# Performance work log

Hardware: AMD Instinct MI355X
Metric: run time of the kernel (lower is better)

The kernel has to match this reference:

```python
import math
import jax, jax.numpy as jnp
import numpy as np

N_HEADS = 16
D_EMBED = 1024
D_HEAD = D_EMBED // N_HEADS


def setup_inputs() -> dict:
    key = jax.random.key(0)
    k1, k2, k3, k4, k5 = jax.random.split(key, 5)
    B, S, D = 4, 2048, D_EMBED
    scale = 1.0 / math.sqrt(D)
    return {
        "x": jax.random.normal(k1, (B, S, D), dtype=jnp.float32),
        "in_proj_w": jax.random.normal(k2, (3 * D, D), dtype=jnp.float32) * scale,
        "in_proj_b": jax.random.normal(k3, (3 * D,), dtype=jnp.float32) * 0.02,
        "out_proj_w": jax.random.normal(k4, (D, D), dtype=jnp.float32) * scale,
        "out_proj_b": jax.random.normal(k5, (D,), dtype=jnp.float32) * 0.02,
        "causal_mask": 0,
    }


def reference(x, in_proj_w, in_proj_b, out_proj_w, out_proj_b, causal_mask):
    B, S, D = x.shape
    # in_proj: torch Linear -> x @ W^T + b, then chunk into q,k,v
    qkv = x @ in_proj_w.T + in_proj_b              # [B,S,3D]
    q, k, v = jnp.split(qkv, 3, axis=-1)
    # [B,S,D] -> [B,H,S,d]
    def heads(t):
        return t.reshape(B, S, N_HEADS, D_HEAD).transpose(0, 2, 1, 3)
    q, k, v = heads(q), heads(k), heads(v)
    weight = jnp.einsum("bhsd,bhtd->bhst", q, k)   # [B,H,S,S] materialized scores
    if causal_mask:
        mask = jnp.triu(jnp.ones((S, S), dtype=bool), k=1)
        weight = jnp.where(mask, -jnp.inf, weight)
    weight = jax.nn.softmax(weight / math.sqrt(D_HEAD), axis=-1)
    out = jnp.einsum("bhst,bhtd->bhsd", weight, v)  # [B,H,S,d]
    out = out.transpose(0, 2, 1, 3).reshape(B, S, D)
    return out @ out_proj_w.T + out_proj_b
```

## Files before the change

kernel.cpp:

```cpp
#include <hip/hip_runtime.h>

typedef unsigned short u16;
typedef _Float16 h8 __attribute__((ext_vector_type(8)));
typedef __fp16 fp16x2 __attribute__((ext_vector_type(2)));
typedef float f32x4 __attribute__((ext_vector_type(4)));

constexpr int B_ = 4, S_ = 2048, D_ = 1024, H_ = 16;

__device__ __forceinline__ void async16(const void* g, void* l) {
  __builtin_amdgcn_global_load_lds(
      (const __attribute__((address_space(1))) void*)g,
      (__attribute__((address_space(3))) void*)l, 16, 0, 0);
}

__device__ __forceinline__ unsigned pk2(float a, float b) {
  union { fp16x2 h; unsigned u; } c;
  c.h = __builtin_amdgcn_cvt_pkrtz(a, b);
  return c.u;
}

__global__ __launch_bounds__(256) void cvt_kernel(
    const float* __restrict__ src, _Float16* __restrict__ dst, int n)
{
  const int i = (blockIdx.x * 256 + threadIdx.x) * 4;
  if (i >= n) return;
  const float4 v = *(const float4*)(src + i);
  uint2 o;
  o.x = pk2(v.x, v.y);
  o.y = pk2(v.z, v.w);
  *(uint2*)(dst + i) = o;
}

template<bool OUT_HALF>
__global__ __launch_bounds__(256, 2) void gemm_wide(
    const _Float16* __restrict__ A, const _Float16* __restrict__ Bw,
    const float* __restrict__ bias, void* __restrict__ Cout,
    int M, int N, int K)
{
  __shared__ __align__(16) _Float16 sA[2][4096];
  __shared__ __align__(16) _Float16 sB[2][8192];

  const int tid = threadIdx.x;
  const int lane = tid & 63, w = tid >> 6;
  const int wm = w & 1, wn = w >> 1;
  const int m0 = blockIdx.y * 128, n0 = blockIdx.x * 256;

  const int sr = 16 * w + (lane & 15);
  const int ss = lane >> 4;
  const _Float16* gA1 = A + (size_t)(m0 + sr) * K + 8 * ss;
  const _Float16* gA2 = gA1 + (size_t)64 * K;
  const _Float16* gB1 = Bw + (size_t)(n0 + sr) * K + 8 * ss;

  const f32x4 zf = {0.f, 0.f, 0.f, 0.f};
  f32x4 acc[4][8];
#pragma unroll
  for (int i = 0; i < 4; ++i)
#pragma unroll
    for (int j = 0; j < 8; ++j) acc[i][j] = zf;

  async16(gA1, &sA[0][w * 512]);
  async16(gA2, &sA[0][(w + 4) * 512]);
#pragma unroll
  for (int t = 0; t < 4; ++t)
    async16(gB1 + (size_t)(64 * t) * K, &sB[0][(w + 4 * t) * 512]);

  const int NIT = K >> 5;
  for (int it = 0; it < NIT; ++it) {
    const int cur = it & 1;
    __syncthreads();
    if (it + 1 < NIT) {
      const int kn = (it + 1) << 5;
      async16(gA1 + kn, &sA[cur ^ 1][w * 512]);
      async16(gA2 + kn, &sA[cur ^ 1][(w + 4) * 512]);
#pragma unroll
      for (int t = 0; t < 4; ++t)
        async16(gB1 + (size_t)(64 * t) * K + kn, &sB[cur ^ 1][(w + 4 * t) * 512]);
    }

    h8 fa[4], fb[8];
#pragma unroll
    for (int i = 0; i < 4; ++i)
      fa[i] = *(const h8*)&sA[cur][((wm * 4 + i) << 9) + (lane << 3)];
#pragma unroll
    for (int j = 0; j < 8; ++j)
      fb[j] = *(const h8*)&sB[cur][((wn * 8 + j) << 9) + (lane << 3)];
#pragma unroll
    for (int i = 0; i < 4; ++i)
#pragma unroll
      for (int j = 0; j < 8; ++j)
        acc[i][j] = __builtin_amdgcn_mfma_f32_16x16x32_f16(fa[i], fb[j], acc[i][j], 0, 0, 0);
  }

  const int g = lane >> 4, cc = lane & 15;
#pragma unroll
  for (int j = 0; j < 8; ++j) {
    const int col = n0 + (wn * 8 + j) * 16 + cc;
    const float bv = bias[col];
#pragma unroll
    for (int i = 0; i < 4; ++i) {
      const int rowb = m0 + (wm * 4 + i) * 16 + g * 4;
#pragma unroll
      for (int r = 0; r < 4; ++r) {
        const float v = acc[i][j][r] + bv;
        if constexpr (OUT_HALF)
          ((_Float16*)Cout)[(size_t)(rowb + r) * N + col] = (_Float16)v;
        else
          ((float*)Cout)[(size_t)(rowb + r) * N + col] = v;
      }
    }
  }
}

template<bool OUT_HALF>
__global__ __launch_bounds__(256) void gemm_f16(
    const _Float16* __restrict__ A, const _Float16* __restrict__ Bw,
    const float* __restrict__ bias, void* __restrict__ Cout,
    int M, int N, int K)
{
  __shared__ __align__(16) _Float16 sA[2][4096];
  __shared__ __align__(16) _Float16 sB[2][4096];

  const int tid = threadIdx.x;
  const int lane = tid & 63, w = tid >> 6;
  const int wm = w & 1, wn = w >> 1;
  const int m0 = blockIdx.y * 128, n0 = blockIdx.x * 128;

  const int sr = 16 * w + (lane & 15);
  const int ss = lane >> 4;
  const _Float16* gA1 = A + (size_t)(m0 + sr) * K + 8 * ss;
  const _Float16* gA2 = gA1 + (size_t)64 * K;
  const _Float16* gB1 = Bw + (size_t)(n0 + sr) * K + 8 * ss;
  const _Float16* gB2 = gB1 + (size_t)64 * K;

  const f32x4 zf = {0.f, 0.f, 0.f, 0.f};
  f32x4 acc[4][4];
#pragma unroll
  for (int i = 0; i < 4; ++i)
#pragma unroll
    for (int j = 0; j < 4; ++j) acc[i][j] = zf;

  async16(gA1, &sA[0][w * 512]);
  async16(gA2, &sA[0][(w + 4) * 512]);
  async16(gB1, &sB[0][w * 512]);
  async16(gB2, &sB[0][(w + 4) * 512]);

  const int NIT = K >> 5;
  for (int it = 0; it < NIT; ++it) {
    const int cur = it & 1;
    __syncthreads();
    if (it + 1 < NIT) {
      const int kn = (it + 1) << 5;
      async16(gA1 + kn, &sA[cur ^ 1][w * 512]);
      async16(gA2 + kn, &sA[cur ^ 1][(w + 4) * 512]);
      async16(gB1 + kn, &sB[cur ^ 1][w * 512]);
      async16(gB2 + kn, &sB[cur ^ 1][(w + 4) * 512]);
    }

    h8 fa[4], fb[4];
#pragma unroll
    for (int i = 0; i < 4; ++i) {
      fa[i] = *(const h8*)&sA[cur][((wm * 4 + i) << 9) + (lane << 3)];
      fb[i] = *(const h8*)&sB[cur][((wn * 4 + i) << 9) + (lane << 3)];
    }
#pragma unroll
    for (int i = 0; i < 4; ++i)
#pragma unroll
      for (int j = 0; j < 4; ++j)
        acc[i][j] = __builtin_amdgcn_mfma_f32_16x16x32_f16(fa[i], fb[j], acc[i][j], 0, 0, 0);
  }

  const int g = lane >> 4, cc = lane & 15;
#pragma unroll
  for (int j = 0; j < 4; ++j) {
    const int col = n0 + (wn * 4 + j) * 16 + cc;
    const float bv = bias[col];
#pragma unroll
    for (int i = 0; i < 4; ++i) {
      const int rowb = m0 + (wm * 4 + i) * 16 + g * 4;
#pragma unroll
      for (int r = 0; r < 4; ++r) {
        const float v = acc[i][j][r] + bv;
        if constexpr (OUT_HALF)
          ((_Float16*)Cout)[(size_t)(rowb + r) * N + col] = (_Float16)v;
        else
          ((float*)Cout)[(size_t)(rowb + r) * N + col] = v;
      }
    }
  }
}

__global__ __launch_bounds__(256) void transpose_v(
    const u16* __restrict__ qkv, u16* __restrict__ vT)
{
  __shared__ u16 T[64 * 73];
  const int tid = threadIdx.x;
  const int bh = blockIdx.y, s0 = blockIdx.x * 64;
  const int b = bh >> 4, h = bh & 15;
#pragma unroll
  for (int t = 0; t < 2; ++t) {
    const int c = tid + t * 256, r = c >> 3, cs = c & 7;
    union { int4 v; u16 s[8]; } u;
    u.v = *(const int4*)(qkv + (size_t)(b * S_ + s0 + r) * 3072 + 2048 + h * 64 + 8 * cs);
#pragma unroll
    for (int i = 0; i < 8; ++i) T[r * 73 + 8 * cs + i] = u.s[i];
  }
  __syncthreads();
#pragma unroll
  for (int t = 0; t < 2; ++t) {
    const int c = tid + t * 256, rd = c >> 3, ss = c & 7;
    union { int4 v; u16 s[8]; } u;
#pragma unroll
    for (int i = 0; i < 8; ++i) u.s[i] = T[(8 * ss + i) * 73 + rd];
    *(int4*)(vT + (size_t)(bh * 64 + rd) * S_ + s0 + 8 * ss) = u.v;
  }
}

__global__ __launch_bounds__(128, 2) void attn_f16(
    const _Float16* __restrict__ qkv, const _Float16* __restrict__ vT,
    _Float16* __restrict__ attnO, const int* __restrict__ causal_ptr)
{
  __shared__ __align__(16) _Float16 sQP[9216];
  __shared__ __align__(16) _Float16 sK[4096];
  __shared__ __align__(16) _Float16 sV[4096];

  const int tid = threadIdx.x, lane = tid & 63, w = tid >> 6;
  const int q4 = lane >> 4, cc = lane & 15;
  const int bh = blockIdx.y, b = bh >> 4, h = bh & 15;
  const int q0 = blockIdx.x * 128;
  const int causal = causal_ptr[0];

  const int rr = lane & 15, sc8 = lane >> 4;

#pragma unroll
  for (int tt = 0; tt < 4; ++tt) {
    const int t = 4 * w + tt;
#pragma unroll
    for (int sh = 0; sh < 2; ++sh) {
      const _Float16* g = qkv + (size_t)(b * S_ + q0 + 16 * t + rr) * 3072 + h * 64 + 8 * (4 * sh + sc8);
      async16(g, &sQP[t * 1024 + sh * 512]);
    }
  }
  __syncthreads();

  h8 qf[4][2];
#pragma unroll
  for (int m = 0; m < 4; ++m)
#pragma unroll
    for (int kk = 0; kk < 2; ++kk) {
      h8 v = *(const h8*)&sQP[((4 * w + m) << 10) + (kk << 9) + (lane << 3)];
      qf[m][kk] = v * (_Float16)0.18033688f;
    }

  h8 ones;
#pragma unroll
  for (int i = 0; i < 8; ++i) ones[i] = (_Float16)1.0f;

  const int wp = w * 4608;

  const f32x4 zf = {0.f, 0.f, 0.f, 0.f};
  f32x4 oa[4][4], lac[4];
#pragma unroll
  for (int m = 0; m < 4; ++m) {
    lac[m] = zf;
#pragma unroll
    for (int nt = 0; nt < 4; ++nt) oa[m][nt] = zf;
  }

  const int nit = causal ? (q0 / 64 + 2) : (S_ / 64);

  for (int it = 0; it < nit; ++it) {
    const int j0 = it * 64;
    __syncthreads();
#pragma unroll
    for (int tt = 0; tt < 2; ++tt) {
      const int t = 2 * w + tt;
#pragma unroll
      for (int sh = 0; sh < 2; ++sh) {
        const _Float16* gk = qkv + (size_t)(b * S_ + j0 + 16 * t + rr) * 3072 + 1024 + h * 64 + 8 * (4 * sh + sc8);
        const _Float16* gv = vT + (size_t)(bh * 64 + 16 * t + rr) * S_ + j0 + 8 * (4 * sh + sc8);
        async16(gk, &sK[t * 1024 + sh * 512]);
        async16(gv, &sV[t * 1024 + sh * 512]);
      }
    }
    __syncthreads();

#pragma unroll
    for (int nt = 0; nt < 4; ++nt) {
      const h8 kf0 = *(const h8*)&sK[(nt << 10) + (lane << 3)];
      const h8 kf1 = *(const h8*)&sK[(nt << 10) + 512 + (lane << 3)];
      f32x4 sc[4];
#pragma unroll
      for (int m = 0; m < 4; ++m) {
        sc[m] = __builtin_amdgcn_mfma_f32_16x16x32_f16(kf0, qf[m][0], zf, 0, 0, 0);
        sc[m] = __builtin_amdgcn_mfma_f32_16x16x32_f16(kf1, qf[m][1], sc[m], 0, 0, 0);
      }
      if (causal) {
#pragma unroll
        for (int m = 0; m < 4; ++m)
#pragma unroll
          for (int r = 0; r < 4; ++r)
            if ((j0 + nt * 16 + q4 * 4 + r) > (q0 + 64 * w + m * 16 + cc))
              sc[m][r] = -1.0e30f;
      }
#pragma unroll
      for (int m = 0; m < 4; ++m) {
        uint2 pk;
        pk.x = pk2(exp2f(sc[m][0]), exp2f(sc[m][1]));
        pk.y = pk2(exp2f(sc[m][2]), exp2f(sc[m][3]));
        *(uint2*)&sQP[wp + (m * 16 + cc) * 72 + nt * 16 + q4 * 4] = pk;
      }
    }

    asm volatile("s_waitcnt lgkmcnt(0)" ::: "memory");

    h8 pf0[4], pf1[4];
#pragma unroll
    for (int m = 0; m < 4; ++m) {
      pf0[m] = *(const h8*)&sQP[wp + (m * 16 + cc) * 72 + q4 * 8];
      pf1[m] = *(const h8*)&sQP[wp + (m * 16 + cc) * 72 + 32 + q4 * 8];
    }

#pragma unroll
    for (int m = 0; m < 4; ++m) {
      lac[m] = __builtin_amdgcn_mfma_f32_16x16x32_f16(pf0[m], ones, lac[m], 0, 0, 0);
      lac[m] = __builtin_amdgcn_mfma_f32_16x16x32_f16(pf1[m], ones, lac[m], 0, 0, 0);
    }
#pragma unroll
    for (int nt = 0; nt < 4; ++nt) {
      const h8 vf0 = *(const h8*)&sV[(nt << 10) + (lane << 3)];
      const h8 vf1 = *(const h8*)&sV[(nt << 10) + 512 + (lane << 3)];
#pragma unroll
      for (int m = 0; m < 4; ++m) {
        oa[m][nt] = __builtin_amdgcn_mfma_f32_16x16x32_f16(pf0[m], vf0, oa[m][nt], 0, 0, 0);
        oa[m][nt] = __builtin_amdgcn_mfma_f32_16x16x32_f16(pf1[m], vf1, oa[m][nt], 0, 0, 0);
      }
    }
  }

#pragma unroll
  for (int m = 0; m < 4; ++m) {
    float inv[4];
#pragma unroll
    for (int r = 0; r < 4; ++r) inv[r] = 1.0f / lac[m][r];
#pragma unroll
    for (int nt = 0; nt < 4; ++nt) {
      const int col = h * 64 + nt * 16 + cc;
#pragma unroll
      for (int r = 0; r < 4; ++r) {
        const int row = b * S_ + q0 + 64 * w + m * 16 + q4 * 4 + r;
        attnO[(size_t)row * D_ + col] = (_Float16)(oa[m][nt][r] * inv[r]);
      }
    }
  }
}

extern "C" void kernel_launch(void* const* d_in, const int* in_sizes, int n_in,
                              void* d_out, int out_size, void* d_ws, size_t ws_size,
                              hipStream_t stream)
{
  const float* x  = (const float*)d_in[0];
  const float* wi = (const float*)d_in[1];
  const float* bi = (const float*)d_in[2];
  const float* wo = (const float*)d_in[3];
  const float* bo = (const float*)d_in[4];
  const int* causal = (const int*)d_in[5];

  _Float16* xh   = (_Float16*)d_ws;
  _Float16* wih  = xh + 8388608;
  _Float16* woh  = wih + 3145728;
  _Float16* qkvb = woh + 1048576;
  _Float16* vT   = qkvb + 25165824;
  _Float16* attn = vT + 8388608;

  const int M = B_ * S_;

  cvt_kernel<<<8192, 256, 0, stream>>>(x, xh, M * D_);
  cvt_kernel<<<3072, 256, 0, stream>>>(wi, wih, 3 * D_ * D_);
  cvt_kernel<<<1024, 256, 0, stream>>>(wo, woh, D_ * D_);

  gemm_wide<true><<<dim3(12, 64), 256, 0, stream>>>(
      xh, wih, bi, qkvb, M, 3 * D_, D_);

  transpose_v<<<dim3(32, 64), 256, 0, stream>>>((const u16*)qkvb, (u16*)vT);

  attn_f16<<<dim3(16, 64), 128, 0, stream>>>(qkvb, vT, attn, causal);

  gemm_f16<false><<<dim3(8, 64), 256, 0, stream>>>(
      attn, woh, bo, d_out, M, D_, D_);
}
```

Baseline: 356.0 us.

## Widen attention blocks to 256 queries and merge fp32-to-fp16 conversion kernels

Attention blocks now use four waves over 256 queries instead of two waves over 128, so each K/V tile staged in LDS is shared by twice as many queries. Each wave loads one K/V subtile per iteration, and Q is read straight from global memory into registers instead of going through LDS. The three conversion launches are merged into one kernel that selects its source by index range, cutting launch overhead. Costs are fewer blocks in flight (512), larger P scratch in LDS, and a tighter occupancy target of three blocks per CU.

```diff
diff --git a/kernel.cpp b/kernel.cpp
--- a/kernel.cpp
+++ b/kernel.cpp
@@ -19,16 +19,21 @@
   return c.u;
 }
 
-__global__ __launch_bounds__(256) void cvt_kernel(
-    const float* __restrict__ src, _Float16* __restrict__ dst, int n)
+__global__ __launch_bounds__(256) void cvt3_kernel(
+    const float* __restrict__ x, const float* __restrict__ wi,
+    const float* __restrict__ wo, _Float16* __restrict__ xh,
+    _Float16* __restrict__ wih, _Float16* __restrict__ woh)
 {
   const int i = (blockIdx.x * 256 + threadIdx.x) * 4;
-  if (i >= n) return;
-  const float4 v = *(const float4*)(src + i);
+  const float* s; _Float16* d; int off;
+  if (i < 8388608)       { s = x;  d = xh;  off = i; }
+  else if (i < 11534336) { s = wi; d = wih; off = i - 8388608; }
+  else                   { s = wo; d = woh; off = i - 11534336; }
+  const float4 v = *(const float4*)(s + off);
   uint2 o;
   o.x = pk2(v.x, v.y);
   o.y = pk2(v.z, v.w);
-  *(uint2*)(dst + i) = o;
+  *(uint2*)(d + off) = o;
 }
 
 template<bool OUT_HALF>
@@ -215,40 +220,30 @@
   }
 }
 
-__global__ __launch_bounds__(128, 2) void attn_f16(
+__global__ __launch_bounds__(256, 3) void attn_f16(
     const _Float16* __restrict__ qkv, const _Float16* __restrict__ vT,
     _Float16* __restrict__ attnO, const int* __restrict__ causal_ptr)
 {
-  __shared__ __align__(16) _Float16 sQP[9216];
+  __shared__ __align__(16) _Float16 sP[18432];
   __shared__ __align__(16) _Float16 sK[4096];
   __shared__ __align__(16) _Float16 sV[4096];
 
   const int tid = threadIdx.x, lane = tid & 63, w = tid >> 6;
   const int q4 = lane >> 4, cc = lane & 15;
   const int bh = blockIdx.y, b = bh >> 4, h = bh & 15;
-  const int q0 = blockIdx.x * 128;
+  const int q0 = blockIdx.x * 256;
   const int causal = causal_ptr[0];
 
   const int rr = lane & 15, sc8 = lane >> 4;
 
-#pragma unroll
-  for (int tt = 0; tt < 4; ++tt) {
-    const int t = 4 * w + tt;
-#pragma unroll
-    for (int sh = 0; sh < 2; ++sh) {
-      const _Float16* g = qkv + (size_t)(b * S_ + q0 + 16 * t + rr) * 3072 + h * 64 + 8 * (4 * sh + sc8);
-      async16(g, &sQP[t * 1024 + sh * 512]);
-    }
-  }
-  __syncthreads();
-
   h8 qf[4][2];
 #pragma unroll
   for (int m = 0; m < 4; ++m)
 #pragma unroll
     for (int kk = 0; kk < 2; ++kk) {
-      h8 v = *(const h8*)&sQP[((4 * w + m) << 10) + (kk << 9) + (lane << 3)];
-      qf[m][kk] = v * (_Float16)0.18033688f;
+      const _Float16* gq = qkv + (size_t)(b * S_ + q0 + 64 * w + 16 * m + cc) * 3072
+                         + h * 64 + kk * 32 + 8 * q4;
+      qf[m][kk] = *(const h8*)gq * (_Float16)0.18033688f;
     }
 
   h8 ones;
@@ -266,22 +261,18 @@
     for (int nt = 0; nt < 4; ++nt) oa[m][nt] = zf;
   }
 
-  const int nit = causal ? (q0 / 64 + 2) : (S_ / 64);
+  const _Float16* gK = qkv + (size_t)(b * S_ + 16 * w + rr) * 3072 + 1024 + h * 64 + 8 * sc8;
+  const _Float16* gV = vT + ((size_t)bh * 64 + 16 * w + rr) * S_ + 8 * sc8;
+
+  const int nit = causal ? (q0 / 64 + 4) : (S_ / 64);
 
   for (int it = 0; it < nit; ++it) {
     const int j0 = it * 64;
     __syncthreads();
-#pragma unroll
-    for (int tt = 0; tt < 2; ++tt) {
-      const int t = 2 * w + tt;
-#pragma unroll
-      for (int sh = 0; sh < 2; ++sh) {
-        const _Float16* gk = qkv + (size_t)(b * S_ + j0 + 16 * t + rr) * 3072 + 1024 + h * 64 + 8 * (4 * sh + sc8);
-        const _Float16* gv = vT + (size_t)(bh * 64 + 16 * t + rr) * S_ + j0 + 8 * (4 * sh + sc8);
-        async16(gk, &sK[t * 1024 + sh * 512]);
-        async16(gv, &sV[t * 1024 + sh * 512]);
-      }
-    }
+    async16(gK + (size_t)j0 * 3072, &sK[w * 1024]);
+    async16(gK + (size_t)j0 * 3072 + 32, &sK[w * 1024 + 512]);
+    async16(gV + j0, &sV[w * 1024]);
+    async16(gV + j0 + 32, &sV[w * 1024 + 512]);
     __syncthreads();
 
 #pragma unroll
@@ -307,7 +298,7 @@
         uint2 pk;
         pk.x = pk2(exp2f(sc[m][0]), exp2f(sc[m][1]));
         pk.y = pk2(exp2f(sc[m][2]), exp2f(sc[m][3]));
-        *(uint2*)&sQP[wp + (m * 16 + cc) * 72 + nt * 16 + q4 * 4] = pk;
+        *(uint2*)&sP[wp + (m * 16 + cc) * 72 + nt * 16 + q4 * 4] = pk;
       }
     }
 
@@ -316,8 +307,8 @@
     h8 pf0[4], pf1[4];
 #pragma unroll
     for (int m = 0; m < 4; ++m) {
-      pf0[m] = *(const h8*)&sQP[wp + (m * 16 + cc) * 72 + q4 * 8];
-      pf1[m] = *(const h8*)&sQP[wp + (m * 16 + cc) * 72 + 32 + q4 * 8];
+      pf0[m] = *(const h8*)&sP[wp + (m * 16 + cc) * 72 + q4 * 8];
+      pf1[m] = *(const h8*)&sP[wp + (m * 16 + cc) * 72 + 32 + q4 * 8];
     }
 
 #pragma unroll
@@ -374,16 +365,14 @@
 
   const int M = B_ * S_;
 
-  cvt_kernel<<<8192, 256, 0, stream>>>(x, xh, M * D_);
-  cvt_kernel<<<3072, 256, 0, stream>>>(wi, wih, 3 * D_ * D_);
-  cvt_kernel<<<1024, 256, 0, stream>>>(wo, woh, D_ * D_);
+  cvt3_kernel<<<12288, 256, 0, stream>>>(x, wi, wo, xh, wih, woh);
 
   gemm_wide<true><<<dim3(12, 64), 256, 0, stream>>>(
       xh, wih, bi, qkvb, M, 3 * D_, D_);
 
   transpose_v<<<dim3(32, 64), 256, 0, stream>>>((const u16*)qkvb, (u16*)vT);
 
-  attn_f16<<<dim3(16, 64), 128, 0, stream>>>(qkvb, vT, attn, causal);
+  attn_f16<<<dim3(8, 64), 256, 0, stream>>>(qkvb, vT, attn, causal);
 
   gemm_f16<false><<<dim3(8, 64), 256, 0, stream>>>(
       attn, woh, bo, d_out, M, D_, D_);
```

After: 358.5 us. Within noise of the previous version (+0.7%).
